# Kernel tuning notes

Hardware: AMD Instinct MI355X
Metric: run time of the kernel (lower is better)

Reference implementation:

```python
import jax, jax.numpy as jnp
import numpy as np

B, ME, R, N, HSZ, V, L, NHEADS = 32, 384, 128, 512, 500, 1000, 2, 4


def _ln(x, g, b, eps=1e-5):
    mu = jnp.mean(x, axis=-1, keepdims=True)
    var = jnp.mean((x - mu) ** 2, axis=-1, keepdims=True)
    return (x - mu) / jnp.sqrt(var + eps) * g + b


def setup_inputs() -> dict:
    key = jax.random.key(0)
    ks = jax.random.split(key, 12)
    ent_vec = jax.random.normal(ks[0], (B, ME, HSZ), jnp.float32)
    entity_num = jax.random.randint(ks[1], (B,), 1, ME + 1)
    rels = jax.random.randint(ks[2], (B, R), 0, V)
    sizes = entity_num + R  # real graph size per sample (<= N)
    idx = jnp.arange(N)
    valid = idx[None, :] < sizes[:, None]
    adj = jax.random.uniform(ks[3], (B, N, N)) < 0.3
    adj = adj & valid[:, None, :] & valid[:, :, None]
    adj = adj | jnp.eye(N, dtype=bool)[None]  # keep diagonal so no all-masked row
    adj = adj.astype(jnp.int32)
    rel_embed = jax.random.normal(ks[4], (V, HSZ)) * (2.0 / (V + HSZ)) ** 0.5  # xavier_normal

    def w(k, shape):
        return (jax.random.normal(k, shape) * 0.03).astype(jnp.float32)

    Wq = w(ks[5], (L, HSZ, HSZ)); Wk = w(ks[6], (L, HSZ, HSZ))
    Wv = w(ks[7], (L, HSZ, HSZ)); Wo = w(ks[8], (L, HSZ, HSZ))
    W1 = w(ks[9], (L, HSZ, 4 * HSZ)); W2 = w(ks[10], (L, 4 * HSZ, HSZ))
    zH = jnp.zeros((L, HSZ), jnp.float32)
    return dict(
        ent_vec=ent_vec, entity_num=entity_num, rels=rels, adj=adj,
        rel_embed=rel_embed,
        Wq=Wq, bq=zH, Wk=Wk, bk=zH, Wv=Wv, bv=zH, Wo=Wo, bo=zH,
        W1=W1, b1=jnp.zeros((L, 4 * HSZ), jnp.float32), W2=W2, b2=zH,
        ln1_g=jnp.ones((L, HSZ), jnp.float32), ln1_b=zH,
        ln2_g=jnp.ones((L, HSZ), jnp.float32), ln2_b=zH,
        prelu_a=jnp.full((L, 4 * HSZ), 0.25, jnp.float32),
    )


def reference(ent_vec, entity_num, rels, adj, rel_embed,
              Wq, bq, Wk, bk, Wv, bv, Wo, bo,
              W1, b1, W2, b2, ln1_g, ln1_b, ln2_g, ln2_b, prelu_a):
    Bb, Me, H = ent_vec.shape
    Rr = rels.shape[1]
    Nn = adj.shape[1]
    Ll = Wq.shape[0]
    dh = H // NHEADS
    idx = jnp.arange(Nn)

    # query_graph = concat(ent_vec[i][:entity_num[i]], rel_embed(rels[i])), padded to N
    is_ent = idx[None, :] < entity_num[:, None]
    eidx = jnp.minimum(idx[None, :], Me - 1)
    ent_part = jnp.take_along_axis(ent_vec, eidx[:, :, None], axis=1)  # (B,N,H)
    ridx = jnp.clip(idx[None, :] - entity_num[:, None], 0, Rr - 1)
    rel_ids = jnp.take_along_axis(rels, ridx, axis=1)  # (B,N)
    rel_part = rel_embed[rel_ids]  # (B,N,H)
    nodes = jnp.where(is_ent[:, :, None], ent_part, rel_part)
    sizes = entity_num + Rr
    validm = idx[None, :] < sizes[:, None]
    nodes = nodes * validm[:, :, None]

    attn_mask = adj != 0  # original masks where adj == 0
    scale = 1.0 / jnp.sqrt(jnp.float32(dh))
    for l in range(Ll):
        kv = jax.lax.stop_gradient(nodes)  # key_graph is detached in original
        q = (nodes @ Wq[l] + bq[l]).reshape(Bb, Nn, NHEADS, dh)
        k = (kv @ Wk[l] + bk[l]).reshape(Bb, Nn, NHEADS, dh)
        v = (kv @ Wv[l] + bv[l]).reshape(Bb, Nn, NHEADS, dh)
        s = jnp.einsum('bqhd,bkhd->bhqk', q, k) * scale
        s = jnp.where(attn_mask[:, None], s, jnp.float32(-1e9))
        a = jax.nn.softmax(s, axis=-1)
        ctx = jnp.einsum('bhqk,bkhd->bqhd', a, v).reshape(Bb, Nn, H)
        o = ctx @ Wo[l] + bo[l]
        t = _ln(o, ln1_g[l], ln1_b[l])
        h1 = t @ W1[l] + b1[l]
        h1 = jnp.where(h1 > 0, h1, prelu_a[l] * h1)  # PReLU, per-channel
        f = h1 @ W2[l] + b2[l]
        nodes = _ln(f + t, ln2_g[l], ln2_b[l])

    node_emb = nodes * validm[:, :, None]  # original pads graphs with zeros
    gidx = jnp.broadcast_to(entity_num[:, None, None], (Bb, 1, H))
    glob = jnp.take_along_axis(nodes, gidx, axis=1)[:, 0]  # query_graph[entity_num[i]]
    out_mask = idx[None, :] <= sizes[:, None]  # faithful '<=' as in original
    return glob, node_emb, out_mask
```

## Files before the change

kernel.cpp:

```cpp
#include <hip/hip_runtime.h>

#define BB 32
#define MEE 384
#define RRELS 128
#define NNODES 512
#define HSZ 500
#define DHEAD 125
#define NHEADS_ 4
#define HID 2000
#define NLAYER 2

#define KP 512
#define HIDP 2048

typedef unsigned short ushort_t;
typedef __attribute__((ext_vector_type(8))) short bf16x8;
typedef __attribute__((ext_vector_type(4))) float f32x4;
typedef __attribute__((ext_vector_type(4))) short s16x4;

static __device__ __forceinline__ unsigned short f2bf(float x) {
    unsigned u = __float_as_uint(x);
    u = u + 0x7fff + ((u >> 16) & 1);
    return (unsigned short)(u >> 16);
}
static __device__ __forceinline__ float bf2f(unsigned short b) {
    return __uint_as_float((unsigned)b << 16);
}

static __device__ __forceinline__ void gload_lds16(const ushort_t* g, ushort_t* l) {
    __builtin_amdgcn_global_load_lds(
        (const __attribute__((address_space(1))) void*)g,
        (__attribute__((address_space(3))) void*)l, 16, 0, 0);
}

__global__ __launch_bounds__(256) void build_nodes_k(
    const float* __restrict__ ent_vec, const int* __restrict__ entity_num,
    const int* __restrict__ rels, const float* __restrict__ rel_embed,
    ushort_t* __restrict__ xb)
{
    int b = blockIdx.x / NNODES;
    int n = blockIdx.x % NNODES;
    int e = entity_num[b];
    const float* src = nullptr;
    if (n < e)               src = ent_vec + ((size_t)b * MEE + n) * HSZ;
    else if (n < e + RRELS)  src = rel_embed + (size_t)rels[b * RRELS + (n - e)] * HSZ;
    ushort_t* xd = xb + ((size_t)b * NNODES + n) * KP;
    for (int d = threadIdx.x; d < KP; d += 256)
        xd[d] = (src && d < HSZ) ? f2bf(src[d]) : 0;
}

__global__ __launch_bounds__(256) void adj_bits_k(
    const int* __restrict__ adj, unsigned int* __restrict__ bits)
{
    int gw = (blockIdx.x * 256 + threadIdx.x) >> 6;
    int lane = threadIdx.x & 63;
    int v = adj[(size_t)gw * 64 + lane];
    unsigned long long mk = __ballot(v != 0);
    if (lane == 0)  bits[gw * 2]     = (unsigned int)mk;
    if (lane == 32) bits[gw * 2 + 1] = (unsigned int)(mk >> 32);
}

__global__ __launch_bounds__(256) void wcvt_all_k(
    const float* __restrict__ pWq, const float* __restrict__ pWk,
    const float* __restrict__ pWv, const float* __restrict__ pWo,
    const float* __restrict__ pW1, const float* __restrict__ pW2,
    ushort_t* __restrict__ wqkv, ushort_t* __restrict__ wo,
    ushort_t* __restrict__ w1, ushort_t* __restrict__ w2)
{
    int idx = blockIdx.x * 256 + threadIdx.x;
    if (idx < 786432) {
        int sub = idx / 262144, r = idx % 262144;
        int n = r / 512, k = r % 512;
        const float* W = sub == 0 ? pWq : (sub == 1 ? pWk : pWv);
        wqkv[idx] = (k < 500 && n < 500) ? f2bf(W[k * 500 + n]) : 0;
    } else if (idx < 1048576) {
        int r = idx - 786432; int n = r / 512, k = r % 512;
        wo[r] = (k < 500 && n < 500) ? f2bf(pWo[k * 500 + n]) : 0;
    } else if (idx < 2097152) {
        int r = idx - 1048576; int n = r / 512, k = r % 512;
        w1[r] = (k < 500 && n < 2000) ? f2bf(pW1[k * 2000 + n]) : 0;
    } else if (idx < 3145728) {
        int r = idx - 2097152; int n = r / 2048, k = r % 2048;
        w2[r] = (k < 2000 && n < 500) ? f2bf(pW2[k * 500 + n]) : 0;
    }
}

__global__ __launch_bounds__(256, 2) void gemm_mfma_k(
    const ushort_t* __restrict__ A, const ushort_t* __restrict__ Bt,
    const float* __restrict__ bias0, const float* __restrict__ bias1,
    const float* __restrict__ bias2,
    ushort_t* __restrict__ outB, ushort_t* __restrict__ outK,
    ushort_t* __restrict__ outV,
    int M, int Np, int Kp, int Nreal,
    const float* __restrict__ prelu, int mode)
{
    __shared__ ushort_t Al[2][128 * 32];
    __shared__ ushort_t Bl[2][128 * 32];

    const int nwg = gridDim.x * gridDim.y;
    const int bid = blockIdx.y * gridDim.x + blockIdx.x;
    const int swz = (bid & 7) * (nwg >> 3) + (bid >> 3);
    const int bm = (swz / gridDim.x) * 128;
    const int bn = (swz % gridDim.x) * 128;

    const int tid = threadIdx.x;
    const int wid = tid >> 6, lane = tid & 63;
    const int wr = wid >> 1, wc = wid & 1;
    const int lr = lane & 15, lk = lane >> 4;

    f32x4 acc[4][4];
#pragma unroll
    for (int i = 0; i < 4; ++i)
#pragma unroll
        for (int j = 0; j < 4; ++j)
#pragma unroll
            for (int r = 0; r < 4; ++r) acc[i][j][r] = 0.f;

    const int srow = tid >> 2;
    const int skseg = (tid & 3) * 8;
    const ushort_t* Ag0 = A + (size_t)(bm + srow) * Kp + skseg;
    const ushort_t* Ag1 = A + (size_t)(bm + 64 + srow) * Kp + skseg;
    const ushort_t* Bg0 = Bt + (size_t)(bn + srow) * Kp + skseg;
    const ushort_t* Bg1 = Bt + (size_t)(bn + 64 + srow) * Kp + skseg;

    auto stage = [&](int bi, int k0) {
        gload_lds16(Ag0 + k0, &Al[bi][wid * 512]);
        gload_lds16(Ag1 + k0, &Al[bi][2048 + wid * 512]);
        gload_lds16(Bg0 + k0, &Bl[bi][wid * 512]);
        gload_lds16(Bg1 + k0, &Bl[bi][2048 + wid * 512]);
    };

    stage(0, 0);
    __syncthreads();
    int cur = 0;

    for (int k0 = 0; k0 < Kp; k0 += 32) {
        if (k0 + 32 < Kp) stage(cur ^ 1, k0 + 32);

        bf16x8 af[4], bfr[4];
#pragma unroll
        for (int mi = 0; mi < 4; ++mi)
            af[mi] = *(const bf16x8*)&Al[cur][(wr * 64 + mi * 16 + lr) * 32 + lk * 8];
#pragma unroll
        for (int ni = 0; ni < 4; ++ni)
            bfr[ni] = *(const bf16x8*)&Bl[cur][(wc * 64 + ni * 16 + lr) * 32 + lk * 8];
        __builtin_amdgcn_s_setprio(1);
#pragma unroll
        for (int mi = 0; mi < 4; ++mi)
#pragma unroll
            for (int ni = 0; ni < 4; ++ni)
                acc[mi][ni] = __builtin_amdgcn_mfma_f32_16x16x32_bf16(
                    af[mi], bfr[ni], acc[mi][ni], 0, 0, 0);
        __builtin_amdgcn_s_setprio(0);

        __syncthreads();
        cur ^= 1;
    }

    if (mode == 1) {
#pragma unroll
        for (int ni = 0; ni < 4; ++ni) {
            int col = bn + wc * 64 + ni * 16 + lr;
            int reg = col >> 9, c = col & 511;
            bool cok = c < 500;
            int hh, dh;
            if (cok) { hh = c / 125; dh = c - hh * 125; }
            else     { hh = (c - 500) / 3; dh = 125 + (c - 500) % 3; }
            const float* bp = reg == 0 ? bias0 : (reg == 1 ? bias1 : bias2);
            float bv = cok ? bp[c] : 0.f;
#pragma unroll
            for (int mi = 0; mi < 4; ++mi) {
                int row0 = bm + wr * 64 + mi * 16 + lk * 4;
                int b_ = row0 >> 9, n0 = row0 & 511;
                size_t bh = (size_t)b_ * 4 + hh;
                if (reg == 2) {
                    s16x4 pk;
#pragma unroll
                    for (int r = 0; r < 4; ++r) {
                        float val = acc[mi][ni][r] + bv;
                        pk[r] = cok ? (short)f2bf(val) : (short)0;
                    }
                    *(s16x4*)&outV[(bh * 128 + dh) * 512 + n0] = pk;
                } else {
                    ushort_t* dst = reg == 0 ? outB : outK;
#pragma unroll
                    for (int r = 0; r < 4; ++r) {
                        float val = acc[mi][ni][r] + bv;
                        dst[(bh * 512 + n0 + r) * 128 + dh] = cok ? f2bf(val) : 0;
                    }
                }
            }
        }
    } else {
#pragma unroll
        for (int ni = 0; ni < 4; ++ni) {
            int col = bn + wc * 64 + ni * 16 + lr;
            bool cok = col < Nreal;
            float bv = cok ? bias0[col] : 0.f;
            float pv = (prelu && cok) ? prelu[col] : 0.f;
#pragma unroll
            for (int mi = 0; mi < 4; ++mi) {
                int row0 = bm + wr * 64 + mi * 16 + lk * 4;
#pragma unroll
                for (int r = 0; r < 4; ++r) {
                    int row = row0 + r;
                    float val = acc[mi][ni][r] + bv;
                    if (prelu) val = val > 0.f ? val : pv * val;
                    outB[(size_t)row * Np + col] = cok ? f2bf(val) : 0;
                }
            }
        }
    }
}

#define KTT 64
__global__ __launch_bounds__(256, 2) void attn_mfma_k(
    const ushort_t* __restrict__ qh, const ushort_t* __restrict__ kh,
    const ushort_t* __restrict__ vT, const unsigned int* __restrict__ abits,
    ushort_t* __restrict__ ctxb)
{
    __shared__ ushort_t Kl[2][KTT * 128];
    __shared__ ushort_t Vl[2][128 * KTT];
    __shared__ ushort_t Pl[4][32 * KTT];

    const int bid = blockIdx.x;
    const int wg = (bid & 7) * 64 + (bid >> 3);
    const int qt2 = wg & 3, bh = wg >> 2;
    const int b = bh >> 2, h = bh & 3;
    const int tid = threadIdx.x, wid = tid >> 6, lane = tid & 63;
    const int lr = lane & 15, lk = lane >> 4;
    const int q0 = qt2 * 128 + wid * 32;
    const float scale = 0.08944271909999159f;

    bf16x8 qa[2][4];
#pragma unroll
    for (int t = 0; t < 2; ++t) {
        const ushort_t* qbase = qh + ((size_t)bh * 512 + q0 + t * 16 + lr) * 128;
#pragma unroll
        for (int ks = 0; ks < 4; ++ks)
            qa[t][ks] = *(const bf16x8*)&qbase[ks * 32 + lk * 8];
    }

    f32x4 accO[2][8];
#pragma unroll
    for (int t = 0; t < 2; ++t)
#pragma unroll
        for (int i = 0; i < 8; ++i)
#pragma unroll
            for (int r = 0; r < 4; ++r) accO[t][i][r] = 0.f;
    float m_[2][4], l_[2][4];
#pragma unroll
    for (int t = 0; t < 2; ++t)
#pragma unroll
        for (int r = 0; r < 4; ++r) { m_[t][r] = -3e38f; l_[t][r] = 0.f; }

    const unsigned int* ab = abits + ((size_t)b * NNODES + q0) * 16;

    auto stage = [&](int bi, int kt) {
#pragma unroll
        for (int i = 0; i < 4; ++i) {
            int linear = (wid * 4 + i) * 64 + lane;
            int row = linear >> 4, cc = linear & 15;
            int cs = cc ^ (row & 7);
            gload_lds16(kh + ((size_t)bh * 512 + kt * 64 + row) * 128 + cs * 8,
                        &Kl[bi][(wid * 4 + i) * 512]);
        }
#pragma unroll
        for (int i = 0; i < 4; ++i) {
            int linear = (wid * 4 + i) * 64 + lane;
            int row = linear >> 3, cc = linear & 7;
            int cs = cc ^ (row & 7);
            gload_lds16(vT + ((size_t)bh * 128 + row) * 512 + kt * 64 + cs * 8,
                        &Vl[bi][(wid * 4 + i) * 512]);
        }
    };

    stage(0, 0);
    __syncthreads();
    int cur = 0;

    for (int kt = 0; kt < NNODES / KTT; ++kt) {
        if (kt < NNODES / KTT - 1) stage(cur ^ 1, kt + 1);

        unsigned int mw[2][4][2];
#pragma unroll
        for (int t = 0; t < 2; ++t)
#pragma unroll
            for (int r = 0; r < 4; ++r) {
                int qrow = t * 16 + lk * 4 + r;
                mw[t][r][0] = ab[qrow * 16 + kt * 2];
                mw[t][r][1] = ab[qrow * 16 + kt * 2 + 1];
            }

#pragma unroll
        for (int t = 0; t < 2; ++t) {
            f32x4 accS[4];
#pragma unroll
            for (int ni = 0; ni < 4; ++ni)
#pragma unroll
                for (int r = 0; r < 4; ++r) accS[ni][r] = 0.f;
            __builtin_amdgcn_s_setprio(1);
#pragma unroll
            for (int ks = 0; ks < 4; ++ks) {
#pragma unroll
                for (int ni = 0; ni < 4; ++ni) {
                    int row = ni * 16 + lr;
                    int ch = (ks * 4 + lk) ^ (row & 7);
                    bf16x8 kb = *(const bf16x8*)&Kl[cur][row * 128 + ch * 8];
                    accS[ni] = __builtin_amdgcn_mfma_f32_16x16x32_bf16(
                        qa[t][ks], kb, accS[ni], 0, 0, 0);
                }
            }
            __builtin_amdgcn_s_setprio(0);
#pragma unroll
            for (int r = 0; r < 4; ++r) {
                float s[4];
#pragma unroll
                for (int ni = 0; ni < 4; ++ni) {
                    unsigned int word = mw[t][r][ni >> 1];
                    int bit = (ni & 1) * 16 + lr;
                    bool on = (word >> bit) & 1u;
                    s[ni] = on ? accS[ni][r] * scale : -1e9f;
                }
                float rowmax = fmaxf(fmaxf(s[0], s[1]), fmaxf(s[2], s[3]));
                rowmax = fmaxf(rowmax, __shfl_xor(rowmax, 1));
                rowmax = fmaxf(rowmax, __shfl_xor(rowmax, 2));
                rowmax = fmaxf(rowmax, __shfl_xor(rowmax, 4));
                rowmax = fmaxf(rowmax, __shfl_xor(rowmax, 8));
                float mnew = fmaxf(m_[t][r], rowmax);
                float f = __expf(m_[t][r] - mnew);
                m_[t][r] = mnew;
                float p[4], rs = 0.f;
#pragma unroll
                for (int ni = 0; ni < 4; ++ni) { p[ni] = __expf(s[ni] - mnew); rs += p[ni]; }
                rs += __shfl_xor(rs, 1);
                rs += __shfl_xor(rs, 2);
                rs += __shfl_xor(rs, 4);
                rs += __shfl_xor(rs, 8);
                l_[t][r] = l_[t][r] * f + rs;
#pragma unroll
                for (int di = 0; di < 8; ++di) accO[t][di][r] *= f;
                int q = t * 16 + lk * 4 + r;
#pragma unroll
                for (int ni = 0; ni < 4; ++ni) {
                    int key = ni * 16 + lr;
                    Pl[wid][q * 64 + (((key >> 3) ^ (q & 7)) << 3) + (key & 7)] = f2bf(p[ni]);
                }
            }
        }

#pragma unroll
        for (int t = 0; t < 2; ++t) {
#pragma unroll
            for (int ksp = 0; ksp < 2; ++ksp) {
                int q = t * 16 + lr;
                int k0p = ksp * 32 + lk * 8;
                bf16x8 pa = *(const bf16x8*)&Pl[wid][q * 64 + (((k0p >> 3) ^ (q & 7)) << 3)];
                __builtin_amdgcn_s_setprio(1);
#pragma unroll
                for (int di = 0; di < 8; ++di) {
                    int row = di * 16 + lr;
                    int ch = (ksp * 4 + lk) ^ (row & 7);
                    bf16x8 vb = *(const bf16x8*)&Vl[cur][row * 64 + ch * 8];
                    accO[t][di] = __builtin_amdgcn_mfma_f32_16x16x32_bf16(
                        pa, vb, accO[t][di], 0, 0, 0);
                }
                __builtin_amdgcn_s_setprio(0);
            }
        }
        __syncthreads();
        cur ^= 1;
    }

    float inv[2][4];
#pragma unroll
    for (int t = 0; t < 2; ++t)
#pragma unroll
        for (int r = 0; r < 4; ++r) inv[t][r] = 1.f / l_[t][r];
#pragma unroll
    for (int t = 0; t < 2; ++t)
#pragma unroll
        for (int di = 0; di < 8; ++di) {
            int d = di * 16 + lr;
            if (d < DHEAD) {
#pragma unroll
                for (int r = 0; r < 4; ++r) {
                    int qg = q0 + t * 16 + lk * 4 + r;
                    ctxb[((size_t)b * NNODES + qg) * KP + h * DHEAD + d] =
                        f2bf(accO[t][di][r] * inv[t][r]);
                }
            }
        }
    if (h == 3) {
        int row = q0 + (lane & 31);
        int c0 = 500 + (lane >> 5) * 6;
#pragma unroll
        for (int j = 0; j < 6; ++j)
            ctxb[((size_t)b * NNODES + row) * KP + c0 + j] = 0;
    }
}

__global__ __launch_bounds__(256) void ln_k(
    const ushort_t* __restrict__ x, const ushort_t* __restrict__ res,
    const float* __restrict__ g, const float* __restrict__ bta,
    ushort_t* __restrict__ outB, float* __restrict__ outF)
{
    size_t row = blockIdx.x;
    const unsigned int* xr = (const unsigned int*)(x + row * KP);
    const unsigned int* rr = res ? (const unsigned int*)(res + row * KP) : nullptr;
    int t = threadIdx.x;
    int d0 = 2 * t;
    unsigned int xv = xr[t];
    float v0 = bf2f((unsigned short)(xv & 0xffff));
    float v1 = bf2f((unsigned short)(xv >> 16));
    if (rr) {
        unsigned int rv = rr[t];
        v0 += bf2f((unsigned short)(rv & 0xffff));
        v1 += bf2f((unsigned short)(rv >> 16));
    }
    if (d0 >= HSZ) v0 = 0.f;
    if (d0 + 1 >= HSZ) v1 = 0.f;
    float s = v0 + v1, s2 = v0 * v0 + v1 * v1;

    __shared__ float red[8];
    int wave = t >> 6, lane = t & 63;
    for (int o = 1; o < 64; o <<= 1) { s += __shfl_xor(s, o); s2 += __shfl_xor(s2, o); }
    if (lane == 0) { red[wave] = s; red[4 + wave] = s2; }
    __syncthreads();
    s  = red[0] + red[1] + red[2] + red[3];
    s2 = red[4] + red[5] + red[6] + red[7];
    float mean = s / HSZ;
    float var  = s2 / HSZ - mean * mean;
    float rstd = rsqrtf(var + 1e-5f);

    float o0 = 0.f, o1 = 0.f;
    if (d0 < HSZ)     o0 = (v0 - mean) * rstd * g[d0] + bta[d0];
    if (d0 + 1 < HSZ) o1 = (v1 - mean) * rstd * g[d0 + 1] + bta[d0 + 1];
    unsigned int pk = (unsigned int)f2bf(o0) | ((unsigned int)f2bf(o1) << 16);
    if (d0 >= HSZ) pk = 0;
    else if (d0 + 1 >= HSZ) pk = (unsigned int)f2bf(o0);
    ((unsigned int*)(outB + row * KP))[t] = pk;
    if (outF) {
        if (d0 < HSZ)     outF[row * HSZ + d0] = o0;
        if (d0 + 1 < HSZ) outF[row * HSZ + d0 + 1] = o1;
    }
}

__global__ __launch_bounds__(256) void finalize_k(
    const float* __restrict__ nodes, const int* __restrict__ entity_num,
    float* __restrict__ out)
{
    int b = blockIdx.x / NNODES;
    int n = blockIdx.x % NNODES;
    int e = entity_num[b];
    int size = e + RRELS;
    const float* src = nodes + ((size_t)b * NNODES + n) * HSZ;
    float* ne = out + (size_t)BB * HSZ + ((size_t)b * NNODES + n) * HSZ;
    bool valid = n < size;
    for (int d = threadIdx.x; d < HSZ; d += 256) ne[d] = valid ? src[d] : 0.f;
    if (n == e) {
        float* gl = out + (size_t)b * HSZ;
        for (int d = threadIdx.x; d < HSZ; d += 256) gl[d] = src[d];
    }
    if (threadIdx.x == 0) {
        out[(size_t)BB * HSZ + (size_t)BB * NNODES * HSZ + (size_t)b * NNODES + n] =
            (n <= size) ? 1.f : 0.f;
    }
}

extern "C" void kernel_launch(void* const* d_in, const int* in_sizes, int n_in,
                              void* d_out, int out_size, void* d_ws, size_t ws_size,
                              hipStream_t stream)
{
    const float* ent_vec    = (const float*)d_in[0];
    const int*   entity_num = (const int*)d_in[1];
    const int*   rels       = (const int*)d_in[2];
    const int*   adj        = (const int*)d_in[3];
    const float* rel_embed  = (const float*)d_in[4];
    const float* Wq = (const float*)d_in[5],  *bq = (const float*)d_in[6];
    const float* Wk = (const float*)d_in[7],  *bk = (const float*)d_in[8];
    const float* Wv = (const float*)d_in[9],  *bv = (const float*)d_in[10];
    const float* Wo = (const float*)d_in[11], *bo = (const float*)d_in[12];
    const float* W1 = (const float*)d_in[13], *b1 = (const float*)d_in[14];
    const float* W2 = (const float*)d_in[15], *b2 = (const float*)d_in[16];
    const float* ln1g = (const float*)d_in[17], *ln1b = (const float*)d_in[18];
    const float* ln2g = (const float*)d_in[19], *ln2b = (const float*)d_in[20];
    const float* pa = (const float*)d_in[21];

    const int M = BB * NNODES;
    const size_t SP = (size_t)M * KP;

    ushort_t* Xb   = (ushort_t*)d_ws;
    ushort_t* ctxb = Xb + SP;
    ushort_t* tb   = ctxb + SP;
    ushort_t* ob   = tb + SP;
    ushort_t* fb   = ob + SP;
    ushort_t* h1b  = fb + SP;
    ushort_t* wqkvb = h1b + (size_t)M * HIDP;
    ushort_t* wob  = wqkvb + 3 * KP * KP;
    ushort_t* w1b  = wob + KP * KP;
    ushort_t* w2b  = w1b + (size_t)HIDP * KP;
    float* nodesF  = (float*)(w2b + (size_t)KP * HIDP);

    ushort_t* qh  = h1b;
    ushort_t* kh  = h1b + SP;
    ushort_t* vTb = h1b + 2 * SP;

    unsigned int* abits = (unsigned int*)d_out;

    build_nodes_k<<<BB * NNODES, 256, 0, stream>>>(ent_vec, entity_num, rels, rel_embed, Xb);
    adj_bits_k<<<(BB * NNODES * NNODES) / 64 / 4, 256, 0, stream>>>(adj, abits);

    for (int l = 0; l < NLAYER; ++l) {
        const float* bq_l = bq + (size_t)l * HSZ;
        const float* bk_l = bk + (size_t)l * HSZ;
        const float* bv_l = bv + (size_t)l * HSZ;
        const float* bo_l = bo + (size_t)l * HSZ;
        const float* b1_l = b1 + (size_t)l * HID;
        const float* b2_l = b2 + (size_t)l * HSZ;
        const float* pa_l = pa + (size_t)l * HID;

        wcvt_all_k<<<12288, 256, 0, stream>>>(
            Wq + (size_t)l * HSZ * HSZ, Wk + (size_t)l * HSZ * HSZ,
            Wv + (size_t)l * HSZ * HSZ, Wo + (size_t)l * HSZ * HSZ,
            W1 + (size_t)l * HSZ * HID, W2 + (size_t)l * HID * HSZ,
            wqkvb, wob, w1b, w2b);

        dim3 gQKV(1536 / 128, M / 128);
        gemm_mfma_k<<<gQKV, 256, 0, stream>>>(Xb, wqkvb, bq_l, bk_l, bv_l,
                                              qh, kh, vTb,
                                              M, 1536, KP, HSZ, nullptr, 1);

        attn_mfma_k<<<BB * NHEADS_ * 4, 256, 0, stream>>>(qh, kh, vTb, abits, ctxb);

        dim3 gO(KP / 128, M / 128);
        gemm_mfma_k<<<gO, 256, 0, stream>>>(ctxb, wob, bo_l, nullptr, nullptr,
                                            ob, nullptr, nullptr,
                                            M, KP, KP, HSZ, nullptr, 0);
        ln_k<<<M, 256, 0, stream>>>(ob, nullptr,
                                    ln1g + (size_t)l * HSZ, ln1b + (size_t)l * HSZ,
                                    tb, nullptr);

        dim3 g1(HIDP / 128, M / 128);
        gemm_mfma_k<<<g1, 256, 0, stream>>>(tb, w1b, b1_l, nullptr, nullptr,
                                            h1b, nullptr, nullptr,
                                            M, HIDP, KP, HID, pa_l, 0);
        dim3 g2(KP / 128, M / 128);
        gemm_mfma_k<<<g2, 256, 0, stream>>>(h1b, w2b, b2_l, nullptr, nullptr,
                                            fb, nullptr, nullptr,
                                            M, KP, HIDP, HSZ, nullptr, 0);

        ln_k<<<M, 256, 0, stream>>>(fb, tb,
                                    ln2g + (size_t)l * HSZ, ln2b + (size_t)l * HSZ,
                                    Xb, (l == NLAYER - 1) ? nodesF : nullptr);
    }

    finalize_k<<<BB * NNODES, 256, 0, stream>>>(nodesF, entity_num, (float*)d_out);
}
```

Before: 566.5 us.

## Coalesce weight conversion, stage GEMM epilogue through LDS, drop fp32 nodes copy

The weight conversion now transposes 64x64 tiles through shared memory, replacing the strided per-element gather with float4 reads and 16-byte bf16 writes. The GEMM epilogue stages each half of the output tile in swizzled LDS so that global stores become 16-byte row writes instead of scattered 2-byte stores. The final layer no longer writes a separate fp32 copy of the nodes; finalize reads the bf16 buffer instead, which lowers output precision to bf16. The epilogue adds extra barriers.

After: 560.7 us. No clear change (-1.0%).

```diff
diff --git a/kernel.cpp b/kernel.cpp
--- a/kernel.cpp
+++ b/kernel.cpp
@@ -60,28 +60,51 @@
     if (lane == 32) bits[gw * 2 + 1] = (unsigned int)(mk >> 32);
 }
 
-__global__ __launch_bounds__(256) void wcvt_all_k(
+__global__ __launch_bounds__(256) void wcvt_t_k(
     const float* __restrict__ pWq, const float* __restrict__ pWk,
     const float* __restrict__ pWv, const float* __restrict__ pWo,
     const float* __restrict__ pW1, const float* __restrict__ pW2,
     ushort_t* __restrict__ wqkv, ushort_t* __restrict__ wo,
     ushort_t* __restrict__ w1, ushort_t* __restrict__ w2)
 {
-    int idx = blockIdx.x * 256 + threadIdx.x;
-    if (idx < 786432) {
-        int sub = idx / 262144, r = idx % 262144;
-        int n = r / 512, k = r % 512;
-        const float* W = sub == 0 ? pWq : (sub == 1 ? pWk : pWv);
-        wqkv[idx] = (k < 500 && n < 500) ? f2bf(W[k * 500 + n]) : 0;
-    } else if (idx < 1048576) {
-        int r = idx - 786432; int n = r / 512, k = r % 512;
-        wo[r] = (k < 500 && n < 500) ? f2bf(pWo[k * 500 + n]) : 0;
-    } else if (idx < 2097152) {
-        int r = idx - 1048576; int n = r / 512, k = r % 512;
-        w1[r] = (k < 500 && n < 2000) ? f2bf(pW1[k * 2000 + n]) : 0;
-    } else if (idx < 3145728) {
-        int r = idx - 2097152; int n = r / 2048, k = r % 2048;
-        w2[r] = (k < 2000 && n < 500) ? f2bf(pW2[k * 500 + n]) : 0;
+    __shared__ float T[64][65];
+    int blk = blockIdx.x;
+    const float* W; ushort_t* out; int Kr, Nr, Kpp, tt;
+    if (blk < 192)      { int s = blk >> 6; W = s == 0 ? pWq : (s == 1 ? pWk : pWv);
+                          out = wqkv + s * 262144; Kr = 500; Nr = 500; Kpp = 512; tt = blk & 63; }
+    else if (blk < 256) { W = pWo; out = wo;  Kr = 500;  Nr = 500;  Kpp = 512;  tt = blk - 192; }
+    else if (blk < 512) { W = pW1; out = w1;  Kr = 500;  Nr = 2000; Kpp = 512;  tt = blk - 256; }
+    else                { W = pW2; out = w2;  Kr = 2000; Nr = 500;  Kpp = 2048; tt = blk - 512; }
+    int ntk = Kpp >> 6;
+    int tk = tt % ntk, tn = tt / ntk;
+    int tid = threadIdx.x;
+#pragma unroll
+    for (int p = 0; p < 4; ++p) {
+        int kl = p * 16 + (tid >> 4);
+        int k  = tk * 64 + kl;
+        int nl = (tid & 15) * 4;
+        int n  = tn * 64 + nl;
+        float4 v = make_float4(0.f, 0.f, 0.f, 0.f);
+        if (k < Kr) {
+            if (n + 3 < Nr) v = *(const float4*)&W[(size_t)k * Nr + n];
+            else {
+                if (n     < Nr) v.x = W[(size_t)k * Nr + n];
+                if (n + 1 < Nr) v.y = W[(size_t)k * Nr + n + 1];
+                if (n + 2 < Nr) v.z = W[(size_t)k * Nr + n + 2];
+                if (n + 3 < Nr) v.w = W[(size_t)k * Nr + n + 3];
+            }
+        }
+        T[kl][nl] = v.x; T[kl][nl + 1] = v.y; T[kl][nl + 2] = v.z; T[kl][nl + 3] = v.w;
+    }
+    __syncthreads();
+#pragma unroll
+    for (int p = 0; p < 2; ++p) {
+        int nl  = p * 32 + (tid >> 3);
+        int kl8 = (tid & 7) * 8;
+        bf16x8 o;
+#pragma unroll
+        for (int j = 0; j < 8; ++j) o[j] = (short)f2bf(T[kl8 + j][nl]);
+        *(bf16x8*)&out[(size_t)(tn * 64 + nl) * Kpp + tk * 64 + kl8] = o;
     }
 }
 
@@ -192,22 +215,38 @@
             }
         }
     } else {
-#pragma unroll
-        for (int ni = 0; ni < 4; ++ni) {
-            int col = bn + wc * 64 + ni * 16 + lr;
-            bool cok = col < Nreal;
-            float bv = cok ? bias0[col] : 0.f;
-            float pv = (prelu && cok) ? prelu[col] : 0.f;
-#pragma unroll
-            for (int mi = 0; mi < 4; ++mi) {
-                int row0 = bm + wr * 64 + mi * 16 + lk * 4;
-#pragma unroll
-                for (int r = 0; r < 4; ++r) {
-                    int row = row0 + r;
-                    float val = acc[mi][ni][r] + bv;
-                    if (prelu) val = val > 0.f ? val : pv * val;
-                    outB[(size_t)row * Np + col] = cok ? f2bf(val) : 0;
-                }
+        ushort_t* Cst = &Al[0][0];
+#pragma unroll
+        for (int half = 0; half < 2; ++half) {
+            __syncthreads();
+            if (wr == half) {
+#pragma unroll
+                for (int ni = 0; ni < 4; ++ni) {
+                    int col = wc * 64 + ni * 16 + lr;
+                    int gcol = bn + col;
+                    bool cok = gcol < Nreal;
+                    float bv = cok ? bias0[gcol] : 0.f;
+                    float pv = (prelu && cok) ? prelu[gcol] : 0.f;
+                    int ch = col >> 3, cl = col & 7;
+#pragma unroll
+                    for (int mi = 0; mi < 4; ++mi) {
+#pragma unroll
+                        for (int r = 0; r < 4; ++r) {
+                            int row = mi * 16 + lk * 4 + r;
+                            float val = acc[mi][ni][r] + bv;
+                            if (prelu) val = val > 0.f ? val : pv * val;
+                            Cst[row * 128 + ((ch ^ (row & 7)) << 3) + cl] = cok ? f2bf(val) : 0;
+                        }
+                    }
+                }
+            }
+            __syncthreads();
+#pragma unroll
+            for (int p = 0; p < 4; ++p) {
+                int row = p * 16 + (tid >> 4);
+                int c = tid & 15;
+                bf16x8 v = *(const bf16x8*)&Cst[row * 128 + ((c ^ (row & 7)) << 3)];
+                *(bf16x8*)&outB[(size_t)(bm + half * 64 + row) * Np + bn + c * 8] = v;
             }
         }
     }
@@ -403,7 +442,7 @@
 __global__ __launch_bounds__(256) void ln_k(
     const ushort_t* __restrict__ x, const ushort_t* __restrict__ res,
     const float* __restrict__ g, const float* __restrict__ bta,
-    ushort_t* __restrict__ outB, float* __restrict__ outF)
+    ushort_t* __restrict__ outB)
 {
     size_t row = blockIdx.x;
     const unsigned int* xr = (const unsigned int*)(x + row * KP);
@@ -440,27 +479,23 @@
     if (d0 >= HSZ) pk = 0;
     else if (d0 + 1 >= HSZ) pk = (unsigned int)f2bf(o0);
     ((unsigned int*)(outB + row * KP))[t] = pk;
-    if (outF) {
-        if (d0 < HSZ)     outF[row * HSZ + d0] = o0;
-        if (d0 + 1 < HSZ) outF[row * HSZ + d0 + 1] = o1;
-    }
 }
 
 __global__ __launch_bounds__(256) void finalize_k(
-    const float* __restrict__ nodes, const int* __restrict__ entity_num,
+    const ushort_t* __restrict__ nodes, const int* __restrict__ entity_num,
     float* __restrict__ out)
 {
     int b = blockIdx.x / NNODES;
     int n = blockIdx.x % NNODES;
     int e = entity_num[b];
     int size = e + RRELS;
-    const float* src = nodes + ((size_t)b * NNODES + n) * HSZ;
+    const ushort_t* src = nodes + ((size_t)b * NNODES + n) * KP;
     float* ne = out + (size_t)BB * HSZ + ((size_t)b * NNODES + n) * HSZ;
     bool valid = n < size;
-    for (int d = threadIdx.x; d < HSZ; d += 256) ne[d] = valid ? src[d] : 0.f;
+    for (int d = threadIdx.x; d < HSZ; d += 256) ne[d] = valid ? bf2f(src[d]) : 0.f;
     if (n == e) {
         float* gl = out + (size_t)b * HSZ;
-        for (int d = threadIdx.x; d < HSZ; d += 256) gl[d] = src[d];
+        for (int d = threadIdx.x; d < HSZ; d += 256) gl[d] = bf2f(src[d]);
     }
     if (threadIdx.x == 0) {
         out[(size_t)BB * HSZ + (size_t)BB * NNODES * HSZ + (size_t)b * NNODES + n] =
@@ -500,7 +535,6 @@
     ushort_t* wob  = wqkvb + 3 * KP * KP;
     ushort_t* w1b  = wob + KP * KP;
     ushort_t* w2b  = w1b + (size_t)HIDP * KP;
-    float* nodesF  = (float*)(w2b + (size_t)KP * HIDP);
 
     ushort_t* qh  = h1b;
     ushort_t* kh  = h1b + SP;
@@ -520,7 +554,7 @@
         const float* b2_l = b2 + (size_t)l * HSZ;
         const float* pa_l = pa + (size_t)l * HID;
 
-        wcvt_all_k<<<12288, 256, 0, stream>>>(
+        wcvt_t_k<<<768, 256, 0, stream>>>(
             Wq + (size_t)l * HSZ * HSZ, Wk + (size_t)l * HSZ * HSZ,
             Wv + (size_t)l * HSZ * HSZ, Wo + (size_t)l * HSZ * HSZ,
             W1 + (size_t)l * HSZ * HID, W2 + (size_t)l * HID * HSZ,
@@ -539,7 +573,7 @@
                                             M, KP, KP, HSZ, nullptr, 0);
         ln_k<<<M, 256, 0, stream>>>(ob, nullptr,
                                     ln1g + (size_t)l * HSZ, ln1b + (size_t)l * HSZ,
-                                    tb, nullptr);
+                                    tb);
 
         dim3 g1(HIDP / 128, M / 128);
         gemm_mfma_k<<<g1, 256, 0, stream>>>(tb, w1b, b1_l, nullptr, nullptr,
@@ -552,8 +586,8 @@
 
         ln_k<<<M, 256, 0, stream>>>(fb, tb,
                                     ln2g + (size_t)l * HSZ, ln2b + (size_t)l * HSZ,
-                                    Xb, (l == NLAYER - 1) ? nodesF : nullptr);
-    }
-
-    finalize_k<<<BB * NNODES, 256, 0, stream>>>(nodesF, entity_num, (float*)d_out);
-}
+                                    Xb);
+    }
+
+    finalize_k<<<BB * NNODES, 256, 0, stream>>>(Xb, entity_num, (float*)d_out);
+}
```
